# Optimization experiments

Measured on AMD Instinct MI355X. Metric: run time of the kernel, lower is better.

## Reference

```python
import jax, jax.numpy as jnp
import numpy as np
from jax import lax

B = 16384
NWIRES = 4


def _conv(x, w, b):
    # NCHW conv, stride 1, SAME padding (pad 1 for k=3)
    y = lax.conv_general_dilated(x, w, (1, 1), ((1, 1), (1, 1)),
                                 dimension_numbers=("NCHW", "OIHW", "NCHW"))
    return y + b[None, :, None, None]


def _pool2(x):
    b, c, h, w = x.shape
    return x.reshape(b, c, h // 2, 2, w // 2, 2).max(axis=(3, 5))


def _apply_1q(state, U, wire):
    # state: (B,2,2,2,2) complex; U: (B,2,2) complex
    s = jnp.moveaxis(state, wire + 1, -1)
    s = jnp.einsum("bij,b...j->b...i", U, s)
    return jnp.moveaxis(s, -1, wire + 1)


def _apply_cnot(state, c, t):
    s0 = jnp.take(state, 0, axis=c + 1)
    s1 = jnp.take(state, 1, axis=c + 1)
    ta = t + 1 if t < c else t  # target axis index after removing control axis
    s1 = jnp.flip(s1, axis=ta)
    return jnp.stack([s0, s1], axis=c + 1)


def _ry(th):
    c = jnp.cos(th / 2)
    s = jnp.sin(th / 2)
    U = jnp.stack([jnp.stack([c, -s], -1), jnp.stack([s, c], -1)], -2)
    return U.astype(jnp.complex64)


def _rz(th):
    e = jnp.exp(-0.5j * th.astype(jnp.complex64))
    z = jnp.zeros_like(e)
    return jnp.stack([jnp.stack([e, z], -1), jnp.stack([z, jnp.conj(e)], -1)], -2)


def _rx(th):
    c = jnp.cos(th / 2).astype(jnp.complex64)
    s = jnp.sin(th / 2).astype(jnp.complex64)
    return jnp.stack([jnp.stack([c, -1j * s], -1), jnp.stack([-1j * s, c], -1)], -2)


def _circuit(params):
    # params: (B, 16) -> PauliZ expvals (B, 4)
    b = params.shape[0]
    state = jnp.zeros((b, 16), jnp.complex64).at[:, 0].set(1.0).reshape(b, 2, 2, 2, 2)
    for i in range(NWIRES):
        state = _apply_1q(state, _ry(params[:, 4 * i + 0]), i)
        state = _apply_1q(state, _rz(params[:, 4 * i + 1]), i)
        state = _apply_1q(state, _rx(params[:, 4 * i + 2]), i)
        state = _apply_cnot(state, i, (i + 1) % NWIRES)
    probs = state.real ** 2 + state.imag ** 2  # (B,2,2,2,2)
    zs = []
    for i in range(NWIRES):
        p = probs.sum(axis=tuple(a for a in range(1, 5) if a != i + 1))  # (B,2)
        zs.append(p[:, 0] - p[:, 1])
    return jnp.stack(zs, axis=-1)


def setup_inputs() -> dict:
    key = jax.random.key(0)
    ks = jax.random.split(key, 12)
    d = {}
    d["x"] = jax.random.normal(ks[0], (B, 1, 28, 28), jnp.float32)
    d["conv1_w"] = jax.random.normal(ks[1], (4, 1, 3, 3), jnp.float32) * 0.3
    d["conv1_b"] = jax.random.normal(ks[2], (4,), jnp.float32) * 0.1
    d["conv2_w"] = jax.random.normal(ks[3], (4, 4, 3, 3), jnp.float32) * 0.15
    d["conv2_b"] = jax.random.normal(ks[4], (4,), jnp.float32) * 0.1
    d["pl_w"] = jax.random.normal(ks[5], (16, 196), jnp.float32) * 0.07
    d["pl_b"] = jax.random.normal(ks[6], (16,), jnp.float32) * 0.05
    d["ro_w"] = jax.random.normal(ks[7], (4, 4), jnp.float32) * 0.5
    d["ro_b"] = jax.random.normal(ks[8], (4,), jnp.float32) * 0.1
    d["bn_w"] = jnp.ones((4,), jnp.float32)
    d["bn_b"] = jnp.zeros((4,), jnp.float32)
    return d


def reference(x, conv1_w, conv1_b, conv2_w, conv2_b, pl_w, pl_b, ro_w, ro_b, bn_w, bn_b):
    h = _pool2(jax.nn.relu(_conv(x, conv1_w, conv1_b)))   # (B,4,14,14)
    h = _pool2(jax.nn.relu(_conv(h, conv2_w, conv2_b)))   # (B,4,7,7)
    flat = h.reshape(x.shape[0], -1)                      # (B,196)
    params = flat @ pl_w.T + pl_b                         # (B,16)
    z = _circuit(params)                                  # (B,4)
    out = z @ ro_w.T + ro_b                               # (B,4)
    mean = out.mean(0)
    var = out.var(0)  # biased, matches torch BN training normalization
    return (out - mean) / jnp.sqrt(var + 1e-5) * bn_w + bn_b
```

## Files before the change

kernel.cpp:

```cpp
#include <hip/hip_runtime.h>
#include <math.h>

#define BATCH 16384

typedef float v2f __attribute__((ext_vector_type(2)));
typedef unsigned short u16;
typedef __attribute__((ext_vector_type(8))) short short8;
typedef __attribute__((ext_vector_type(4))) float f32x4;

__device__ __forceinline__ v2f pk_fma(v2f a, v2f b, v2f c) {
  return __builtin_elementwise_fma(a, b, c);
}
__device__ __forceinline__ v2f pk_max(v2f a, v2f b) {
  return __builtin_elementwise_max(a, b);
}

__device__ __forceinline__ unsigned bf2(float lo, float hi) {
  unsigned a = __float_as_uint(lo);
  unsigned b = __float_as_uint(hi);
  a = (a + 0x7fffu + ((a >> 16) & 1u)) >> 16;
  b = (b + 0x7fffu + ((b >> 16) & 1u)) & 0xffff0000u;
  return a | b;
}

__device__ __forceinline__ unsigned cvtpk(float lo, float hi) {
  unsigned r;
  asm("v_cvt_pk_bf16_f32 %0, %1, %2" : "=v"(r) : "v"(lo), "v"(hi));
  return r;
}

__global__ __launch_bounds__(256) void qnat_fused(
    const float* __restrict__ x,
    const float* __restrict__ w1,
    const float* __restrict__ b1,
    const float* __restrict__ w2,
    const float* __restrict__ b2,
    const float* __restrict__ plw,
    const float* __restrict__ plb,
    const float* __restrict__ rw,
    const float* __restrict__ rb,
    float* __restrict__ pre,
    float* __restrict__ stats)
{
  __shared__ __align__(16) unsigned h1cur[4][513];
  __shared__ __align__(16) u16 h2b[16][232];
  __shared__ __align__(16) uint4 plw_tb[28 * 16];
  __shared__ __align__(16) short8 b2ft[128];
  __shared__ float s_red[4][8];

  const int tid = threadIdx.x;
  const int w = tid >> 6;
  const int lane = tid & 63;
  const int base = (blockIdx.x * 4 + w) * 4;

  #pragma unroll
  for (int j = 0; j < 2; j++) {
    int s = tid + 256 * j;
    if (s < 448) {
      int tp = s >> 4;
      int k2 = s & 15;
      uint4 v = make_uint4(0u, 0u, 0u, 0u);
      if (tp < 25) {
        const float4* pr = (const float4*)(plw + k2 * 196);
        float4 a = pr[2 * tp];
        float4 b = (tp < 24) ? pr[2 * tp + 1] : make_float4(0.f, 0.f, 0.f, 0.f);
        v = make_uint4(bf2(a.x, a.y), bf2(a.z, a.w),
                       bf2(b.x, b.y), bf2(b.z, b.w));
      }
      plw_tb[s] = v;
    }
  }

  if (tid < 128) {
    int h = tid >> 6, g = (tid >> 4) & 3, n = tid & 15;
    int co = n >> 2, sy = (n >> 1) & 1, sx = n & 1;
    short8 bv;
    #pragma unroll
    for (int j = 0; j < 8; j++) {
      int s = 32 * h + 8 * g + j;
      int ci = s >> 4, dy = (s >> 2) & 3, dx = s & 3;
      int ry = dy - sy, rx = dx - sx;
      float v = 0.0f;
      if (ry >= 0 && ry < 3 && rx >= 0 && rx < 3)
        v = w2[((co * 4 + ci) * 3 + ry) * 3 + rx];
      bv[j] = (short)(u16)bf2(v, 0.0f);
    }
    b2ft[tid] = bv;
  }

  {
    uint4 z4 = make_uint4(0u, 0u, 0u, 0u);
    uint4* hz = (uint4*)h1cur;
    #pragma unroll
    for (int t = 0; t < 3; t++) {
      int p = tid + 256 * t;
      if (p < 513) hz[p] = z4;
    }
    uint4* hz2 = (uint4*)h2b;
    #pragma unroll
    for (int t = 0; t < 2; t++) {
      int p = tid + 256 * t;
      if (p < 464) hz2[p] = z4;
    }
  }
  __syncthreads();

  const int i = lane >> 2;
  const int q = lane & 3;
  const bool c1act = lane < 56;

  float4 pfa[4], pfb[4];
  float pe0[4], pe1[4];
  #pragma unroll
  for (int r = 0; r < 4; r++) {
    pfa[r] = make_float4(0,0,0,0); pfb[r] = make_float4(0,0,0,0);
    pe0[r] = 0.0f; pe1[r] = 0.0f;
  }

  if (c1act) {
    const float* xb = x + (size_t)base * 784;
    #pragma unroll
    for (int r = 0; r < 4; r++) {
      int row = 2 * i - 1 + r;
      if (0 <= row && row < 28) {
        const float* rp = xb + row * 28;
        pfa[r] = *(const float4*)(rp + 8 * q);
        if (q > 0) pe0[r] = rp[8 * q - 1];
        if (q < 3) {
          pfb[r] = *(const float4*)(rp + 8 * q + 4);
          pe1[r] = rp[8 * q + 8];
        }
      }
    }
  }

  #pragma unroll 1
  for (int it = 0; it < 4; ++it) {
    if (c1act) {
      float win[4][10];
      #pragma unroll
      for (int r = 0; r < 4; r++) {
        win[r][0] = pe0[r];
        win[r][1] = pfa[r].x; win[r][2] = pfa[r].y;
        win[r][3] = pfa[r].z; win[r][4] = pfa[r].w;
        win[r][5] = pfb[r].x; win[r][6] = pfb[r].y;
        win[r][7] = pfb[r].z; win[r][8] = pfb[r].w;
        win[r][9] = pe1[r];
      }
      if (it != 3) {
        const float* xn = x + (size_t)(base + it + 1) * 784;
        #pragma unroll
        for (int r = 0; r < 4; r++) {
          int row = 2 * i - 1 + r;
          pfa[r] = make_float4(0,0,0,0);
          pfb[r] = make_float4(0,0,0,0);
          pe0[r] = 0.0f; pe1[r] = 0.0f;
          if (0 <= row && row < 28) {
            const float* rp = xn + row * 28;
            pfa[r] = *(const float4*)(rp + 8 * q);
            if (q > 0) pe0[r] = rp[8 * q - 1];
            if (q < 3) {
              pfb[r] = *(const float4*)(rp + 8 * q + 4);
              pe1[r] = rp[8 * q + 8];
            }
          }
        }
      }
      v2f P[4][9];
      #pragma unroll
      for (int r = 0; r < 4; r++)
        #pragma unroll
        for (int k = 0; k < 9; k++) P[r][k] = (v2f){win[r][k], win[r][k + 1]};

      u16* hs = (u16*)&h1cur[w][0] + (i + 1) * 16 + 4 * q;
      #pragma unroll
      for (int c = 0; c < 4; c++) {
        const float* wc = w1 + c * 9;
        const v2f bias2 = (v2f){b1[c], b1[c]};
        v2f a0[4], a1[4];
        #pragma unroll
        for (int jj = 0; jj < 4; jj++) { a0[jj] = bias2; a1[jj] = bias2; }
        #pragma unroll
        for (int dy = 0; dy < 3; dy++)
          #pragma unroll
          for (int dx = 0; dx < 3; dx++) {
            const float wv = wc[dy * 3 + dx];
            const v2f wvv = (v2f){wv, wv};
            #pragma unroll
            for (int jj = 0; jj < 4; jj++) {
              a0[jj] = pk_fma(P[dy][2 * jj + dx],     wvv, a0[jj]);
              a1[jj] = pk_fma(P[dy + 1][2 * jj + dx], wvv, a1[jj]);
            }
          }
        float m[4];
        #pragma unroll
        for (int jj = 0; jj < 4; jj++) {
          v2f mm = pk_max(a0[jj], a1[jj]);
          m[jj] = fmaxf(fmaxf(mm.x, mm.y), 0.0f);
        }
        u16* p = hs + c * 256;
        p[1] = (u16)cvtpk(m[0], m[0]);
        if (q < 3) {
          *(unsigned*)(p + 2) = cvtpk(m[1], m[2]);
          p[4] = (u16)cvtpk(m[3], m[3]);
        } else {
          p[2] = (u16)cvtpk(m[1], m[1]);
        }
      }
    }
    __syncthreads();

    {
      const int n2 = lane & 15;
      const int g2 = lane >> 4;
      short8 bfr0 = b2ft[g2 * 16 + n2];
      short8 bfr1 = b2ft[64 + g2 * 16 + n2];
      const float bias = b2[n2 >> 2];
      const int msA = lane & 3;
      const int psA = (lane >> 2) & 3;
      const int ciA = g2 >> 1;
      const int dy0 = 2 * (g2 & 1);
      const unsigned* h1 = &h1cur[0][0];

      for (int G = w; G < 13; G += 4) {
        int p = 4 * G + psA;
        int i2 = (p * 9363) >> 16;
        int j2 = p - 7 * i2;
        int a = msA * 513 + ciA * 128 + (2 * i2 + dy0) * 8 + j2;
        unsigned A0 = h1[a],       A1 = h1[a + 1];
        unsigned A2 = h1[a + 8],   A3 = h1[a + 9];
        short8 av0 = __builtin_bit_cast(short8, make_uint4(A0, A1, A2, A3));
        unsigned B0 = h1[a + 256], B1 = h1[a + 257];
        unsigned B2 = h1[a + 264], B3 = h1[a + 265];
        short8 av1 = __builtin_bit_cast(short8, make_uint4(B0, B1, B2, B3));
        f32x4 acc = {bias, bias, bias, bias};
        acc = __builtin_amdgcn_mfma_f32_16x16x32_bf16(av0, bfr0, acc, 0, 0, 0);
        acc = __builtin_amdgcn_mfma_f32_16x16x32_bf16(av1, bfr1, acc, 0, 0, 0);
        float r0 = acc[0], r1 = acc[1], r2 = acc[2], r3 = acc[3];
        r0 = fmaxf(r0, __shfl_xor(r0, 1, 64)); r0 = fmaxf(r0, __shfl_xor(r0, 2, 64));
        r1 = fmaxf(r1, __shfl_xor(r1, 1, 64)); r1 = fmaxf(r1, __shfl_xor(r1, 2, 64));
        r2 = fmaxf(r2, __shfl_xor(r2, 1, 64)); r2 = fmaxf(r2, __shfl_xor(r2, 2, 64));
        r3 = fmaxf(r3, __shfl_xor(r3, 1, 64)); r3 = fmaxf(r3, __shfl_xor(r3, 2, 64));
        int pst = 4 * G + g2;
        if ((lane & 3) == 0 && pst < 49) {
          int off = 49 * (n2 >> 2) + pst;
          float v0 = fmaxf(r0, 0.0f);
          float v1 = fmaxf(r1, 0.0f);
          float v2 = fmaxf(r2, 0.0f);
          float v3 = fmaxf(r3, 0.0f);
          h2b[it][off]      = (u16)cvtpk(v0, v0);
          h2b[4 + it][off]  = (u16)cvtpk(v1, v1);
          h2b[8 + it][off]  = (u16)cvtpk(v2, v2);
          h2b[12 + it][off] = (u16)cvtpk(v3, v3);
        }
      }
    }
    __syncthreads();
  }

  const int s2 = lane >> 4;
  const int k = lane & 15;

  float cv, sv;
  {
    const int arow = lane & 15;
    const int kg = lane >> 4;
    const short8* ha = (const short8*)&h2b[arow][0];
    const short8* hbw = (const short8*)plw_tb;
    f32x4 acc = {0.f, 0.f, 0.f, 0.f};
    #pragma unroll
    for (int kt = 0; kt < 7; kt++) {
      short8 av = ha[4 * kt + kg];
      short8 bv = hbw[(4 * kt + kg) * 16 + arow];
      acc = __builtin_amdgcn_mfma_f32_16x16x32_bf16(av, bv, acc, 0, 0, 0);
    }
    const int srcl = 16 * w + k;
    float c0 = __shfl(acc[0], srcl, 64);
    float c1 = __shfl(acc[1], srcl, 64);
    float c2 = __shfl(acc[2], srcl, 64);
    float c3 = __shfl(acc[3], srcl, 64);
    float pv = (s2 & 2) ? ((s2 & 1) ? c3 : c2) : ((s2 & 1) ? c1 : c0);
    pv += plb[k];
    __sincosf(pv * 0.5f, &sv, &cv);
  }

  {
    const int l = k;
    const int gb = lane & 48;
    float re = (l == 0) ? 1.0f : 0.0f;
    float im = 0.0f;
    #pragma unroll
    for (int qi = 0; qi < 4; qi++) {
      const int beta = 3 - qi;
      const int m = 1 << beta;
      const int b = (l >> beta) & 1;
      float c = __shfl(cv, gb + 4 * qi, 64), s = __shfl(sv, gb + 4 * qi, 64);
      float pr_ = __shfl_xor(re, m, 64), pi_ = __shfl_xor(im, m, 64);
      float sg = b ? s : -s;
      re = fmaf(c, re, sg * pr_);
      im = fmaf(c, im, sg * pi_);
      c = __shfl(cv, gb + 4 * qi + 1, 64); s = __shfl(sv, gb + 4 * qi + 1, 64);
      float sz = b ? s : -s;
      float nr = c * re - sz * im;
      float ni = c * im + sz * re;
      re = nr; im = ni;
      c = __shfl(cv, gb + 4 * qi + 2, 64); s = __shfl(sv, gb + 4 * qi + 2, 64);
      pr_ = __shfl_xor(re, m, 64); pi_ = __shfl_xor(im, m, 64);
      nr = fmaf(c, re, s * pi_);
      ni = fmaf(c, im, -s * pr_);
      re = nr; im = ni;
      const int tm = 1 << (3 - ((qi + 1) & 3));
      float fr = __shfl_xor(re, tm, 64), fi = __shfl_xor(im, tm, 64);
      if (b) { re = fr; im = fi; }
    }
    float pr2 = re * re + im * im;
    float z0 = ((l >> 3) & 1) ? -pr2 : pr2;
    float z1 = ((l >> 2) & 1) ? -pr2 : pr2;
    float z2 = ((l >> 1) & 1) ? -pr2 : pr2;
    float z3 = (l & 1) ? -pr2 : pr2;
    #pragma unroll
    for (int off = 8; off >= 1; off >>= 1) {
      z0 += __shfl_xor(z0, off, 64);
      z1 += __shfl_xor(z1, off, 64);
      z2 += __shfl_xor(z2, off, 64);
      z3 += __shfl_xor(z3, off, 64);
    }
    float as0 = 0.f, as1 = 0.f, as2 = 0.f, as3 = 0.f;
    float aq0 = 0.f, aq1 = 0.f, aq2 = 0.f, aq3 = 0.f;
    if (l == 0) {
      float o0 = fmaf(rw[0],  z0, fmaf(rw[1],  z1, fmaf(rw[2],  z2, fmaf(rw[3],  z3, rb[0]))));
      float o1 = fmaf(rw[4],  z0, fmaf(rw[5],  z1, fmaf(rw[6],  z2, fmaf(rw[7],  z3, rb[1]))));
      float o2 = fmaf(rw[8],  z0, fmaf(rw[9],  z1, fmaf(rw[10], z2, fmaf(rw[11], z3, rb[2]))));
      float o3 = fmaf(rw[12], z0, fmaf(rw[13], z1, fmaf(rw[14], z2, fmaf(rw[15], z3, rb[3]))));
      *(float4*)(pre + (size_t)(base + s2) * 4) = make_float4(o0, o1, o2, o3);
      as0 = o0; aq0 = o0 * o0;
      as1 = o1; aq1 = o1 * o1;
      as2 = o2; aq2 = o2 * o2;
      as3 = o3; aq3 = o3 * o3;
    }
    #pragma unroll
    for (int off = 32; off >= 16; off >>= 1) {
      as0 += __shfl_down(as0, off, 64); aq0 += __shfl_down(aq0, off, 64);
      as1 += __shfl_down(as1, off, 64); aq1 += __shfl_down(aq1, off, 64);
      as2 += __shfl_down(as2, off, 64); aq2 += __shfl_down(aq2, off, 64);
      as3 += __shfl_down(as3, off, 64); aq3 += __shfl_down(aq3, off, 64);
    }
    if (lane == 0) {
      s_red[w][0] = as0; s_red[w][4] = aq0;
      s_red[w][1] = as1; s_red[w][5] = aq1;
      s_red[w][2] = as2; s_red[w][6] = aq2;
      s_red[w][3] = as3; s_red[w][7] = aq3;
    }
  }
  __syncthreads();
  if (tid < 8) {
    float v = s_red[0][tid] + s_red[1][tid] + s_red[2][tid] + s_red[3][tid];
    atomicAdd(&stats[tid], v);
  }
}

__global__ __launch_bounds__(256) void qnat_bn(
    float* __restrict__ pre,
    const float* __restrict__ stats,
    const float* __restrict__ bnw,
    const float* __restrict__ bnb)
{
  int idx = blockIdx.x * 256 + threadIdx.x;
  int c = idx & 3;
  float mean = stats[c] * (1.0f / BATCH);
  float ex2 = stats[4 + c] * (1.0f / BATCH);
  float var = ex2 - mean * mean;
  float inv = rsqrtf(var + 1e-5f);
  pre[idx] = (pre[idx] - mean) * inv * bnw[c] + bnb[c];
}

extern "C" void kernel_launch(void* const* d_in, const int* in_sizes, int n_in,
                              void* d_out, int out_size, void* d_ws, size_t ws_size,
                              hipStream_t stream) {
  const float* x   = (const float*)d_in[0];
  const float* w1  = (const float*)d_in[1];
  const float* b1  = (const float*)d_in[2];
  const float* w2  = (const float*)d_in[3];
  const float* b2  = (const float*)d_in[4];
  const float* plw = (const float*)d_in[5];
  const float* plb = (const float*)d_in[6];
  const float* rw  = (const float*)d_in[7];
  const float* rb  = (const float*)d_in[8];
  const float* bnw = (const float*)d_in[9];
  const float* bnb = (const float*)d_in[10];

  float* out   = (float*)d_out;
  float* stats = (float*)d_ws;

  hipMemsetAsync(stats, 0, 8 * sizeof(float), stream);
  qnat_fused<<<BATCH / 16, 256, 0, stream>>>(x, w1, b1, w2, b2, plw, plb, rw, rb, out, stats);
  qnat_bn<<<(BATCH * 4) / 256, 256, 0, stream>>>(out, stats, bnw, bnb);
}
```

Measured before the change: 133.3 us.

## Make conv2 per-wave on own sample, drop per-iteration block barriers

Conv2 MFMA work is reassigned so each wave processes only the sample whose conv1 output it wrote itself, covering all 49 pooled positions in four unrolled tiles instead of splitting tiles across waves. Because no cross-wave data flows inside the loop, the two __syncthreads per iteration are removed and a single barrier follows the loop. The h1cur row stride grows from 513 to 560 and the zero-fill range is extended to match. The reassignment also changes the MFMA M-dimension mapping (positions rather than samples), so the store indexing is rewritten. The risk is load imbalance and LDS bank conflicts from the new stride and mapping.

After: 131.0 us. Within noise of the previous version (-1.7%).

```diff
diff --git a/kernel.cpp b/kernel.cpp
--- a/kernel.cpp
+++ b/kernel.cpp
@@ -42,7 +42,7 @@
     float* __restrict__ pre,
     float* __restrict__ stats)
 {
-  __shared__ __align__(16) unsigned h1cur[4][513];
+  __shared__ __align__(16) unsigned h1cur[4][560];
   __shared__ __align__(16) u16 h2b[16][232];
   __shared__ __align__(16) uint4 plw_tb[28 * 16];
   __shared__ __align__(16) short8 b2ft[128];
@@ -94,7 +94,7 @@
     #pragma unroll
     for (int t = 0; t < 3; t++) {
       int p = tid + 256 * t;
-      if (p < 513) hz[p] = z4;
+      if (p < 560) hz[p] = z4;
     }
     uint4* hz2 = (uint4*)h2b;
     #pragma unroll
@@ -208,25 +208,24 @@
         }
       }
     }
-    __syncthreads();
 
     {
       const int n2 = lane & 15;
       const int g2 = lane >> 4;
-      short8 bfr0 = b2ft[g2 * 16 + n2];
-      short8 bfr1 = b2ft[64 + g2 * 16 + n2];
+      const short8 bfr0 = b2ft[g2 * 16 + n2];
+      const short8 bfr1 = b2ft[64 + g2 * 16 + n2];
       const float bias = b2[n2 >> 2];
-      const int msA = lane & 3;
-      const int psA = (lane >> 2) & 3;
       const int ciA = g2 >> 1;
       const int dy0 = 2 * (g2 & 1);
-      const unsigned* h1 = &h1cur[0][0];
-
-      for (int G = w; G < 13; G += 4) {
-        int p = 4 * G + psA;
+      const unsigned* h1 = &h1cur[w][0];
+      u16* hq = &h2b[4 * w + it][0];
+
+      #pragma unroll
+      for (int t = 0; t < 4; t++) {
+        int p = 16 * t + n2;
         int i2 = (p * 9363) >> 16;
         int j2 = p - 7 * i2;
-        int a = msA * 513 + ciA * 128 + (2 * i2 + dy0) * 8 + j2;
+        int a = ciA * 128 + (2 * i2 + dy0) * 8 + j2;
         unsigned A0 = h1[a],       A1 = h1[a + 1];
         unsigned A2 = h1[a + 8],   A3 = h1[a + 9];
         short8 av0 = __builtin_bit_cast(short8, make_uint4(A0, A1, A2, A3));
@@ -241,22 +240,19 @@
         r1 = fmaxf(r1, __shfl_xor(r1, 1, 64)); r1 = fmaxf(r1, __shfl_xor(r1, 2, 64));
         r2 = fmaxf(r2, __shfl_xor(r2, 1, 64)); r2 = fmaxf(r2, __shfl_xor(r2, 2, 64));
         r3 = fmaxf(r3, __shfl_xor(r3, 1, 64)); r3 = fmaxf(r3, __shfl_xor(r3, 2, 64));
-        int pst = 4 * G + g2;
-        if ((lane & 3) == 0 && pst < 49) {
-          int off = 49 * (n2 >> 2) + pst;
-          float v0 = fmaxf(r0, 0.0f);
-          float v1 = fmaxf(r1, 0.0f);
-          float v2 = fmaxf(r2, 0.0f);
-          float v3 = fmaxf(r3, 0.0f);
-          h2b[it][off]      = (u16)cvtpk(v0, v0);
-          h2b[4 + it][off]  = (u16)cvtpk(v1, v1);
-          h2b[8 + it][off]  = (u16)cvtpk(v2, v2);
-          h2b[12 + it][off] = (u16)cvtpk(v3, v3);
-        }
-      }
-    }
-    __syncthreads();
-  }
+        if ((lane & 3) == 0) {
+          int co = n2 >> 2;
+          int prow = 16 * t + 4 * g2;
+          u16* hc = hq + 49 * co;
+          if (prow < 49)     { float v0 = fmaxf(r0, 0.0f); hc[prow]     = (u16)cvtpk(v0, v0); }
+          if (prow + 1 < 49) { float v1 = fmaxf(r1, 0.0f); hc[prow + 1] = (u16)cvtpk(v1, v1); }
+          if (prow + 2 < 49) { float v2 = fmaxf(r2, 0.0f); hc[prow + 2] = (u16)cvtpk(v2, v2); }
+          if (prow + 3 < 49) { float v3 = fmaxf(r3, 0.0f); hc[prow + 3] = (u16)cvtpk(v3, v3); }
+        }
+      }
+    }
+  }
+  __syncthreads();
 
   const int s2 = lane >> 4;
   const int k = lane & 15;
```
